# Kernel tuning notes

Measured on AMD Instinct MI355X. Metric: run time of the kernel, lower is better.

## Reference

```python
import jax, jax.numpy as jnp
import numpy as np

N_LAYERS = 3
N_NODES = 100000
N_EDGES = 1600000
D = 32


def setup_inputs() -> dict:
    key = jax.random.key(0)
    k1, k2, k3, k4 = jax.random.split(key, 4)
    edge_row = jax.random.randint(k1, (N_EDGES,), 0, N_NODES, dtype=jnp.int64 if jax.config.jax_enable_x64 else jnp.int32)
    edge_col = jax.random.randint(k2, (N_EDGES,), 0, N_NODES, dtype=edge_row.dtype)
    edge_val = jax.random.uniform(k3, (N_EDGES,), dtype=jnp.float32)
    x = jax.random.normal(k4, (N_NODES, D), dtype=jnp.float32)
    return {"edge_row": edge_row, "edge_col": edge_col, "edge_val": edge_val, "x": x}


def _spmm(edge_row, edge_col, edge_val, h):
    # y[r] = sum_{edges e with row r} val[e] * h[col[e]]  -- COO SpMM
    msgs = edge_val[:, None] * h[edge_col]  # [E, D]
    return jax.ops.segment_sum(msgs, edge_row, num_segments=N_NODES)


def reference(edge_row, edge_col, edge_val, x):
    # LightGCN propagation: mean over layer-0..n_layers embeddings
    out = x
    acc = x
    for _ in range(N_LAYERS):
        out = _spmm(edge_row, edge_col, edge_val, out)
        acc = acc + out
    return acc / jnp.asarray(N_LAYERS + 1, dtype=x.dtype)
```

## Files before the change

### kernel.cpp

```cpp
#include <hip/hip_runtime.h>


#define NN 100000
#define NE 1600000
#define DD 32
#define CHUNK 4096
#define NCHUNK ((NE + CHUNK - 1) / CHUNK)
#define BROWS 128
#define NBKT ((NN + BROWS - 1) / BROWS)
#define LDSE 3072

__device__ __forceinline__ unsigned f2bf(float f) {
    unsigned u = __float_as_uint(f);
    return (u + 0x7fffu + ((u >> 16) & 1u)) >> 16;
}


__global__ __launch_bounds__(1024) void hist_kernel(
    const int* __restrict__ row, int* __restrict__ H)
{
    __shared__ int cnt[NBKT];
    const int tid = threadIdx.x;
    const int start = blockIdx.x * CHUNK;
    const int n = min(CHUNK, NE - start);
    for (int k = tid; k < NBKT; k += 1024) cnt[k] = 0;
    __syncthreads();
    const int j = tid * 4;
    if (j + 3 < n) {
        int4 r4 = *(const int4*)(row + start + j);
        atomicAdd(&cnt[r4.x >> 7], 1);
        atomicAdd(&cnt[r4.y >> 7], 1);
        atomicAdd(&cnt[r4.z >> 7], 1);
        atomicAdd(&cnt[r4.w >> 7], 1);
    } else {
        for (int k = j; k < n; k++) atomicAdd(&cnt[row[start + k] >> 7], 1);
    }
    __syncthreads();
    int* Hrow = H + (size_t)blockIdx.x * NBKT;
    for (int k = tid; k < NBKT; k += 1024) Hrow[k] = cnt[k];
}


__global__ __launch_bounds__(1024) void scan_tr_kernel(
    const int* __restrict__ H, int* __restrict__ Pt, int* __restrict__ tot)
{
    const int b = blockIdx.x * 16 + (threadIdx.x >> 6);
    if (b >= NBKT) return;
    const int lane = threadIdx.x & 63;
    int run = 0;
    #pragma unroll
    for (int c0 = 0; c0 < NCHUNK; c0 += 64) {
        int c = c0 + lane;
        int v = (c < NCHUNK) ? H[(size_t)c * NBKT + b] : 0;
        int x = v;
        #pragma unroll
        for (int off = 1; off < 64; off <<= 1) {
            int y = __shfl_up(x, off, 64);
            if (lane >= off) x += y;
        }
        if (c < NCHUNK) Pt[(size_t)b * NCHUNK + c] = run + x - v;
        run += __shfl(x, 63, 64);
    }
    if (lane == 0) tot[b] = run;
}


__global__ __launch_bounds__(1024) void scan_buckets_kernel(
    const int* __restrict__ tot, int* __restrict__ bucketbase,
    int* __restrict__ row_ptr)
{
    const int tid = threadIdx.x;
    int v = (tid < NBKT) ? tot[tid] : 0;
    int lane = tid & 63, w = tid >> 6;
    int x = v;
    #pragma unroll
    for (int off = 1; off < 64; off <<= 1) {
        int y = __shfl_up(x, off, 64);
        if (lane >= off) x += y;
    }
    __shared__ int wt[16];
    if (lane == 63) wt[w] = x;
    __syncthreads();
    if (w == 0 && lane < 16) {
        int y = wt[lane];
        #pragma unroll
        for (int off = 1; off < 16; off <<= 1) {
            int z = __shfl_up(y, off, 16);
            if ((lane & 15) >= off) y += z;
        }
        wt[lane] = y;
    }
    __syncthreads();
    int wo = (w > 0) ? wt[w - 1] : 0;
    int excl = x + wo - v;
    if (tid < NBKT) bucketbase[tid] = excl;
    if (tid == NBKT) { bucketbase[NBKT] = NE; row_ptr[NN] = NE; }
}


__global__ __launch_bounds__(1024) void scatter_kernel(
    const int* __restrict__ row, const int* __restrict__ col,
    const float* __restrict__ val, const int* __restrict__ bucketbase,
    const int* __restrict__ Pt, int2* __restrict__ tmp)
{
    __shared__ int cnt[NBKT];
    __shared__ int lbase[NBKT];
    __shared__ int gofs[NBKT];
    __shared__ int wt[16];
    __shared__ int2 recs[CHUNK];
    __shared__ int dest[CHUNK];
    const int tid = threadIdx.x;
    const int start = blockIdx.x * CHUNK;
    const int n = min(CHUNK, NE - start);
    for (int k = tid; k < NBKT; k += 1024) cnt[k] = 0;
    __syncthreads();

    int rrow[CHUNK / 1024], rcol[CHUNK / 1024], rank[CHUNK / 1024];
    float rval[CHUNK / 1024];
    #pragma unroll
    for (int k = 0; k < CHUNK / 1024; k++) {
        int j = k * 1024 + tid;
        if (j < n) {
            int r = row[start + j];
            rrow[k] = r;
            rcol[k] = col[start + j];
            rval[k] = val[start + j];
            rank[k] = atomicAdd(&cnt[r >> 7], 1);
        } else {
            rrow[k] = -1;
        }
    }
    __syncthreads();

    int v = (tid < NBKT) ? cnt[tid] : 0;
    {
        int lane = tid & 63, w = tid >> 6;
        int x = v;
        #pragma unroll
        for (int off = 1; off < 64; off <<= 1) {
            int y = __shfl_up(x, off, 64);
            if (lane >= off) x += y;
        }
        if (lane == 63) wt[w] = x;
        __syncthreads();
        if (w == 0 && lane < 16) {
            int y = wt[lane];
            #pragma unroll
            for (int off = 1; off < 16; off <<= 1) {
                int z = __shfl_up(y, off, 16);
                if ((lane & 15) >= off) y += z;
            }
            wt[lane] = y;
        }
        __syncthreads();
        int excl = x + ((w > 0) ? wt[w - 1] : 0) - v;
        if (tid < NBKT) {
            lbase[tid] = excl;
            gofs[tid] = bucketbase[tid] + Pt[(size_t)tid * NCHUNK + blockIdx.x];
        }
    }
    __syncthreads();

    #pragma unroll
    for (int k = 0; k < CHUNK / 1024; k++) {
        if (rrow[k] >= 0) {
            int b = rrow[k] >> 7;
            int p = lbase[b] + rank[k];
            recs[p] = make_int2(((rrow[k] & 127) << 17) | rcol[k],
                                __float_as_int(rval[k]));
            dest[p] = gofs[b] + rank[k];
        }
    }
    __syncthreads();

    for (int p = tid; p < n; p += 1024)
        tmp[dest[p]] = recs[p];
}


__global__ __launch_bounds__(512) void bucket_sort_kernel(
    const int* __restrict__ bucketbase, const int2* __restrict__ tmp,
    int* __restrict__ row_ptr, int2* __restrict__ edges,
    int* __restrict__ rowperm)
{
    __shared__ int cntw[8][BROWS];
    __shared__ int curw[8][BROWS];
    __shared__ int base[BROWS];
    __shared__ int degsh[BROWS];
    __shared__ int wt2[2];
    __shared__ int2 ed[LDSE];
    const int tid = threadIdx.x;
    const int w   = tid >> 6;
    const int b   = blockIdx.x;
    const int s   = bucketbase[b];
    const int e   = bucketbase[b + 1];
    const int tot = e - s;

    for (int k = tid; k < 8 * BROWS; k += 512) (&cntw[0][0])[k] = 0;
    __syncthreads();

    int2 rc[6];
    #pragma unroll
    for (int k = 0; k < 6; k++) {
        int j = s + k * 512 + tid;
        rc[k] = (j < e && j < s + LDSE) ? tmp[j] : make_int2(-1, 0);
        if (rc[k].x >= 0) atomicAdd(&cntw[w][rc[k].x >> 17], 1);
    }
    if (tot > LDSE)
        for (int j = s + LDSE + tid; j < e; j += 512)
            atomicAdd(&cntw[w][tmp[j].x >> 17], 1);
    __syncthreads();

    int v = 0, x = 0;
    if (tid < BROWS) {
        int d = 0;
        #pragma unroll
        for (int ww = 0; ww < 8; ww++) d += cntw[ww][tid];
        degsh[tid] = d;
        v = d;
        int lane = tid & 63;
        x = v;
        #pragma unroll
        for (int off = 1; off < 64; off <<= 1) {
            int y = __shfl_up(x, off, 64);
            if (lane >= off) x += y;
        }
        if (lane == 63) wt2[tid >> 6] = x;
    }
    __syncthreads();
    if (tid < BROWS) {
        int excl = x + ((tid >> 6) ? wt2[0] : 0) - v;
        base[tid] = excl;
        int r = b * BROWS + tid;
        if (r < NN) row_ptr[r] = s + excl;
        int run = excl;
        #pragma unroll
        for (int ww = 0; ww < 8; ww++) { curw[ww][tid] = run; run += cntw[ww][tid]; }
        int half0 = tid & 64;
        int d = degsh[tid];
        int rank = 0;
        #pragma unroll 8
        for (int j2 = 0; j2 < 64; j2++) {
            int dj = degsh[half0 + j2];
            rank += (dj < d) || (dj == d && (half0 + j2) < tid);
        }
        rowperm[b * BROWS + half0 + rank] = b * BROWS + tid;
    }
    __syncthreads();

    if (tot <= LDSE) {
        #pragma unroll
        for (int k = 0; k < 6; k++) {
            if (rc[k].x >= 0) {
                int pos = atomicAdd(&curw[w][rc[k].x >> 17], 1);
                ed[pos] = make_int2(rc[k].x & 0x1FFFF, rc[k].y);
            }
        }
        __syncthreads();
        for (int k = tid; k < tot; k += 512)
            edges[s + k] = ed[k];
    } else {
        #pragma unroll
        for (int k = 0; k < 6; k++) {
            if (rc[k].x >= 0) {
                int pos = atomicAdd(&curw[w][rc[k].x >> 17], 1);
                edges[s + pos] = make_int2(rc[k].x & 0x1FFFF, rc[k].y);
            }
        }
        for (int j = s + LDSE + tid; j < e; j += 512) {
            int2 rec = tmp[j];
            int pos = atomicAdd(&curw[w][rec.x >> 17], 1);
            edges[s + pos] = make_int2(rec.x & 0x1FFFF, rec.y);
        }
    }
}


__global__ __launch_bounds__(256) void cvt_kernel(
    const float2* __restrict__ xin2, unsigned* __restrict__ hb)
{
    int j = blockIdx.x * 256 + threadIdx.x;
    if (j >= NN * DD / 2) return;
    float2 f = xin2[j];
    hb[j] = f2bf(f.x) | (f2bf(f.y) << 16);
}


template <int MODE>
__global__ __launch_bounds__(256) void spmm_kernel(
    const int* __restrict__ row_ptr, const int2* __restrict__ edges,
    const int* __restrict__ rowperm,
    const uint4* __restrict__ hb4,
    uint4* __restrict__ houtb4,
    const float4* __restrict__ xin4, float4* __restrict__ out4)
{
    const int g0 = blockIdx.x * 64 + (threadIdx.x >> 2);
    const int g = rowperm[g0];
    if (g >= NN) return;
    const int t = threadIdx.x & 3;
    const int s = row_ptr[g];
    const int e = row_ptr[g + 1];

    float acc[8] = {0.f, 0.f, 0.f, 0.f, 0.f, 0.f, 0.f, 0.f};

#define ACC8(W, V)                                                         \
    do {                                                                   \
        acc[0] += (V) * __uint_as_float((W).x << 16);                      \
        acc[1] += (V) * __uint_as_float((W).x & 0xffff0000u);              \
        acc[2] += (V) * __uint_as_float((W).y << 16);                      \
        acc[3] += (V) * __uint_as_float((W).y & 0xffff0000u);              \
        acc[4] += (V) * __uint_as_float((W).z << 16);                      \
        acc[5] += (V) * __uint_as_float((W).z & 0xffff0000u);              \
        acc[6] += (V) * __uint_as_float((W).w << 16);                      \
        acc[7] += (V) * __uint_as_float((W).w & 0xffff0000u);              \
    } while (0)

    int i = s;
    for (; i + 8 <= e; i += 8) {
        int2 a0 = edges[i];
        int2 a1 = edges[i + 1];
        int2 a2 = edges[i + 2];
        int2 a3 = edges[i + 3];
        int2 a4 = edges[i + 4];
        int2 a5 = edges[i + 5];
        int2 a6 = edges[i + 6];
        int2 a7 = edges[i + 7];
        uint4 w0 = hb4[a0.x * 4 + t];
        uint4 w1 = hb4[a1.x * 4 + t];
        uint4 w2 = hb4[a2.x * 4 + t];
        uint4 w3 = hb4[a3.x * 4 + t];
        uint4 w4 = hb4[a4.x * 4 + t];
        uint4 w5 = hb4[a5.x * 4 + t];
        uint4 w6 = hb4[a6.x * 4 + t];
        uint4 w7 = hb4[a7.x * 4 + t];
        ACC8(w0, __int_as_float(a0.y)); ACC8(w1, __int_as_float(a1.y));
        ACC8(w2, __int_as_float(a2.y)); ACC8(w3, __int_as_float(a3.y));
        ACC8(w4, __int_as_float(a4.y)); ACC8(w5, __int_as_float(a5.y));
        ACC8(w6, __int_as_float(a6.y)); ACC8(w7, __int_as_float(a7.y));
    }
    for (; i + 4 <= e; i += 4) {
        int2 a0 = edges[i];
        int2 a1 = edges[i + 1];
        int2 a2 = edges[i + 2];
        int2 a3 = edges[i + 3];
        uint4 w0 = hb4[a0.x * 4 + t];
        uint4 w1 = hb4[a1.x * 4 + t];
        uint4 w2 = hb4[a2.x * 4 + t];
        uint4 w3 = hb4[a3.x * 4 + t];
        ACC8(w0, __int_as_float(a0.y)); ACC8(w1, __int_as_float(a1.y));
        ACC8(w2, __int_as_float(a2.y)); ACC8(w3, __int_as_float(a3.y));
    }
    for (; i < e; ++i) {
        int2 a0 = edges[i];
        uint4 w0 = hb4[a0.x * 4 + t];
        ACC8(w0, __int_as_float(a0.y));
    }
#undef ACC8

    if (MODE == 0 || MODE == 1) {
        uint4 p;
        p.x = f2bf(acc[0]) | (f2bf(acc[1]) << 16);
        p.y = f2bf(acc[2]) | (f2bf(acc[3]) << 16);
        p.z = f2bf(acc[4]) | (f2bf(acc[5]) << 16);
        p.w = f2bf(acc[6]) | (f2bf(acc[7]) << 16);
        houtb4[g * 4 + t] = p;
    }
    const int o = g * 8 + t * 2;
    float4 lo, hi;
    if (MODE == 0) {
        float4 x0 = xin4[o], x1 = xin4[o + 1];
        lo = make_float4(x0.x + acc[0], x0.y + acc[1], x0.z + acc[2], x0.w + acc[3]);
        hi = make_float4(x1.x + acc[4], x1.y + acc[5], x1.z + acc[6], x1.w + acc[7]);
    } else if (MODE == 1) {
        float4 o0 = out4[o], o1 = out4[o + 1];
        lo = make_float4(o0.x + acc[0], o0.y + acc[1], o0.z + acc[2], o0.w + acc[3]);
        hi = make_float4(o1.x + acc[4], o1.y + acc[5], o1.z + acc[6], o1.w + acc[7]);
    } else {
        float4 o0 = out4[o], o1 = out4[o + 1];
        lo = make_float4((o0.x + acc[0]) * 0.25f, (o0.y + acc[1]) * 0.25f,
                         (o0.z + acc[2]) * 0.25f, (o0.w + acc[3]) * 0.25f);
        hi = make_float4((o1.x + acc[4]) * 0.25f, (o1.y + acc[5]) * 0.25f,
                         (o1.z + acc[6]) * 0.25f, (o1.w + acc[7]) * 0.25f);
    }
    out4[o] = lo;
    out4[o + 1] = hi;
}


extern "C" void kernel_launch(void* const* d_in, const int* in_sizes, int n_in,
                              void* d_out, int out_size, void* d_ws, size_t ws_size,
                              hipStream_t stream) {
    const int*   edge_row = (const int*)d_in[0];
    const int*   edge_col = (const int*)d_in[1];
    const float* edge_val = (const float*)d_in[2];
    const float* x        = (const float*)d_in[3];
    float* out = (float*)d_out;

    char* ws = (char*)d_ws;
    int*  H          = (int*)ws;   ws += (((size_t)NCHUNK * NBKT * 4) + 511) & ~511ull;
    int*  Pt         = (int*)ws;   ws += (((size_t)NBKT * NCHUNK * 4) + 511) & ~511ull;
    int*  tot        = (int*)ws;   ws += 4096;
    int*  bucketbase = (int*)ws;   ws += 4096;
    int*  row_ptr    = (int*)ws;   ws += ((size_t)(NN + 1) * 4 + 511) & ~511ull;
    int*  rowperm    = (int*)ws;   ws += (((size_t)NBKT * BROWS * 4) + 511) & ~511ull;
    int2* tmp        = (int2*)ws;  ws += (size_t)NE * 8 + 64;
    int2* edges      = (int2*)ws;  ws += (size_t)NE * 8 + 64;
    unsigned* hb0    = (unsigned*)ws;  ws += (size_t)NN * DD * 2;
    unsigned* hb1    = (unsigned*)ws;  ws += (size_t)NN * DD * 2;

    hist_kernel        <<<NCHUNK, 1024, 0, stream>>>(edge_row, H);
    scan_tr_kernel     <<<(NBKT + 15) / 16, 1024, 0, stream>>>(H, Pt, tot);
    scan_buckets_kernel<<<1, 1024, 0, stream>>>(tot, bucketbase, row_ptr);
    scatter_kernel     <<<NCHUNK, 1024, 0, stream>>>(edge_row, edge_col, edge_val,
                                                     bucketbase, Pt, tmp);
    bucket_sort_kernel <<<NBKT, 512, 0, stream>>>(bucketbase, tmp, row_ptr, edges,
                                                  rowperm);
    cvt_kernel         <<<(NN * DD / 2 + 255) / 256, 256, 0, stream>>>(
                         (const float2*)x, hb0);

    dim3 sp_grid((NN + 63) / 64);
    spmm_kernel<0><<<sp_grid, 256, 0, stream>>>(row_ptr, edges, rowperm,
        (const uint4*)hb0, (uint4*)hb1, (const float4*)x, (float4*)out);
    spmm_kernel<1><<<sp_grid, 256, 0, stream>>>(row_ptr, edges, rowperm,
        (const uint4*)hb1, (uint4*)hb0, (const float4*)x, (float4*)out);
    spmm_kernel<2><<<sp_grid, 256, 0, stream>>>(row_ptr, edges, rowperm,
        (const uint4*)hb0, (uint4*)hb1, (const float4*)x, (float4*)out);
}
```

Baseline: 199.3 us.

## Split bf16 features into two planes and run SpMM per half-feature plane

Stores the bf16 node features as two separate 16-feature planes and launches each SpMM layer twice, once per plane. Within a row, pairs of lanes now split the edges and combine partial sums with a cross-lane shuffle. The goal is a smaller gather working set per pass (a 3.2 MB plane) that fits better in cache. It also drops the per-bucket degree-sorted row permutation. In exchange the edge list is read twice per layer, the number of launches doubles, and half the lanes sit idle during the final writes.

Result: slower. 229.8 us (+15.3%).

```diff
diff --git a/kernel.cpp b/kernel.cpp
--- a/kernel.cpp
+++ b/kernel.cpp
@@ -9,6 +9,7 @@
 #define BROWS 128
 #define NBKT ((NN + BROWS - 1) / BROWS)
 #define LDSE 3072
+#define PLANE_U4 (NN * 2)
 
 __device__ __forceinline__ unsigned f2bf(float f) {
     unsigned u = __float_as_uint(f);
@@ -180,13 +181,10 @@
 
 __global__ __launch_bounds__(512) void bucket_sort_kernel(
     const int* __restrict__ bucketbase, const int2* __restrict__ tmp,
-    int* __restrict__ row_ptr, int2* __restrict__ edges,
-    int* __restrict__ rowperm)
+    int* __restrict__ row_ptr, int2* __restrict__ edges)
 {
     __shared__ int cntw[8][BROWS];
     __shared__ int curw[8][BROWS];
-    __shared__ int base[BROWS];
-    __shared__ int degsh[BROWS];
     __shared__ int wt2[2];
     __shared__ int2 ed[LDSE];
     const int tid = threadIdx.x;
@@ -216,7 +214,6 @@
         int d = 0;
         #pragma unroll
         for (int ww = 0; ww < 8; ww++) d += cntw[ww][tid];
-        degsh[tid] = d;
         v = d;
         int lane = tid & 63;
         x = v;
@@ -230,21 +227,11 @@
     __syncthreads();
     if (tid < BROWS) {
         int excl = x + ((tid >> 6) ? wt2[0] : 0) - v;
-        base[tid] = excl;
         int r = b * BROWS + tid;
         if (r < NN) row_ptr[r] = s + excl;
         int run = excl;
         #pragma unroll
         for (int ww = 0; ww < 8; ww++) { curw[ww][tid] = run; run += cntw[ww][tid]; }
-        int half0 = tid & 64;
-        int d = degsh[tid];
-        int rank = 0;
-        #pragma unroll 8
-        for (int j2 = 0; j2 < 64; j2++) {
-            int dj = degsh[half0 + j2];
-            rank += (dj < d) || (dj == d && (half0 + j2) < tid);
-        }
-        rowperm[b * BROWS + half0 + rank] = b * BROWS + tid;
     }
     __syncthreads();
 
@@ -280,24 +267,25 @@
     const float2* __restrict__ xin2, unsigned* __restrict__ hb)
 {
     int j = blockIdx.x * 256 + threadIdx.x;
-    if (j >= NN * DD / 2) return;
+    if (j >= NN * 16) return;
     float2 f = xin2[j];
-    hb[j] = f2bf(f.x) | (f2bf(f.y) << 16);
+    int nd = j >> 4, ff = j & 15;
+    hb[(ff >> 3) * (NN * 8) + nd * 8 + (ff & 7)] = f2bf(f.x) | (f2bf(f.y) << 16);
 }
 
 
 template <int MODE>
 __global__ __launch_bounds__(256) void spmm_kernel(
     const int* __restrict__ row_ptr, const int2* __restrict__ edges,
-    const int* __restrict__ rowperm,
-    const uint4* __restrict__ hb4,
-    uint4* __restrict__ houtb4,
-    const float4* __restrict__ xin4, float4* __restrict__ out4)
-{
-    const int g0 = blockIdx.x * 64 + (threadIdx.x >> 2);
-    const int g = rowperm[g0];
+    const uint4* __restrict__ hbp,
+    uint4* __restrict__ houtp,
+    const float4* __restrict__ xin4, float4* __restrict__ out4, int fo)
+{
+    const int g = blockIdx.x * 64 + (threadIdx.x >> 2);
     if (g >= NN) return;
-    const int t = threadIdx.x & 3;
+    const int t  = threadIdx.x & 3;
+    const int tp = t >> 1;
+    const int tc = t & 1;
     const int s = row_ptr[g];
     const int e = row_ptr[g + 1];
 
@@ -317,55 +305,42 @@
 
     int i = s;
     for (; i + 8 <= e; i += 8) {
-        int2 a0 = edges[i];
-        int2 a1 = edges[i + 1];
-        int2 a2 = edges[i + 2];
-        int2 a3 = edges[i + 3];
-        int2 a4 = edges[i + 4];
-        int2 a5 = edges[i + 5];
-        int2 a6 = edges[i + 6];
-        int2 a7 = edges[i + 7];
-        uint4 w0 = hb4[a0.x * 4 + t];
-        uint4 w1 = hb4[a1.x * 4 + t];
-        uint4 w2 = hb4[a2.x * 4 + t];
-        uint4 w3 = hb4[a3.x * 4 + t];
-        uint4 w4 = hb4[a4.x * 4 + t];
-        uint4 w5 = hb4[a5.x * 4 + t];
-        uint4 w6 = hb4[a6.x * 4 + t];
-        uint4 w7 = hb4[a7.x * 4 + t];
-        ACC8(w0, __int_as_float(a0.y)); ACC8(w1, __int_as_float(a1.y));
-        ACC8(w2, __int_as_float(a2.y)); ACC8(w3, __int_as_float(a3.y));
-        ACC8(w4, __int_as_float(a4.y)); ACC8(w5, __int_as_float(a5.y));
-        ACC8(w6, __int_as_float(a6.y)); ACC8(w7, __int_as_float(a7.y));
-    }
-    for (; i + 4 <= e; i += 4) {
-        int2 a0 = edges[i];
-        int2 a1 = edges[i + 1];
-        int2 a2 = edges[i + 2];
-        int2 a3 = edges[i + 3];
-        uint4 w0 = hb4[a0.x * 4 + t];
-        uint4 w1 = hb4[a1.x * 4 + t];
-        uint4 w2 = hb4[a2.x * 4 + t];
-        uint4 w3 = hb4[a3.x * 4 + t];
-        ACC8(w0, __int_as_float(a0.y)); ACC8(w1, __int_as_float(a1.y));
-        ACC8(w2, __int_as_float(a2.y)); ACC8(w3, __int_as_float(a3.y));
-    }
-    for (; i < e; ++i) {
-        int2 a0 = edges[i];
-        uint4 w0 = hb4[a0.x * 4 + t];
-        ACC8(w0, __int_as_float(a0.y));
+        int2 r0 = edges[i + 0 + tp];
+        int2 r1 = edges[i + 2 + tp];
+        int2 r2 = edges[i + 4 + tp];
+        int2 r3 = edges[i + 6 + tp];
+        uint4 w0 = hbp[r0.x * 2 + tc];
+        uint4 w1 = hbp[r1.x * 2 + tc];
+        uint4 w2 = hbp[r2.x * 2 + tc];
+        uint4 w3 = hbp[r3.x * 2 + tc];
+        ACC8(w0, __int_as_float(r0.y)); ACC8(w1, __int_as_float(r1.y));
+        ACC8(w2, __int_as_float(r2.y)); ACC8(w3, __int_as_float(r3.y));
+    }
+    for (; i + 2 <= e; i += 2) {
+        int2 r0 = edges[i + tp];
+        uint4 w0 = hbp[r0.x * 2 + tc];
+        ACC8(w0, __int_as_float(r0.y));
+    }
+    if (i < e && tp == 0) {
+        int2 r0 = edges[i];
+        uint4 w0 = hbp[r0.x * 2 + tc];
+        ACC8(w0, __int_as_float(r0.y));
     }
 #undef ACC8
 
+    #pragma unroll
+    for (int k = 0; k < 8; k++) acc[k] += __shfl_xor(acc[k], 2, 64);
+
+    if (t >= 2) return;
     if (MODE == 0 || MODE == 1) {
         uint4 p;
         p.x = f2bf(acc[0]) | (f2bf(acc[1]) << 16);
         p.y = f2bf(acc[2]) | (f2bf(acc[3]) << 16);
         p.z = f2bf(acc[4]) | (f2bf(acc[5]) << 16);
         p.w = f2bf(acc[6]) | (f2bf(acc[7]) << 16);
-        houtb4[g * 4 + t] = p;
-    }
-    const int o = g * 8 + t * 2;
+        houtp[g * 2 + t] = p;
+    }
+    const int o = g * 8 + fo * 4 + t * 2;
     float4 lo, hi;
     if (MODE == 0) {
         float4 x0 = xin4[o], x1 = xin4[o + 1];
@@ -402,7 +377,6 @@
     int*  tot        = (int*)ws;   ws += 4096;
     int*  bucketbase = (int*)ws;   ws += 4096;
     int*  row_ptr    = (int*)ws;   ws += ((size_t)(NN + 1) * 4 + 511) & ~511ull;
-    int*  rowperm    = (int*)ws;   ws += (((size_t)NBKT * BROWS * 4) + 511) & ~511ull;
     int2* tmp        = (int2*)ws;  ws += (size_t)NE * 8 + 64;
     int2* edges      = (int2*)ws;  ws += (size_t)NE * 8 + 64;
     unsigned* hb0    = (unsigned*)ws;  ws += (size_t)NN * DD * 2;
@@ -413,16 +387,26 @@
     scan_buckets_kernel<<<1, 1024, 0, stream>>>(tot, bucketbase, row_ptr);
     scatter_kernel     <<<NCHUNK, 1024, 0, stream>>>(edge_row, edge_col, edge_val,
                                                      bucketbase, Pt, tmp);
-    bucket_sort_kernel <<<NBKT, 512, 0, stream>>>(bucketbase, tmp, row_ptr, edges,
-                                                  rowperm);
-    cvt_kernel         <<<(NN * DD / 2 + 255) / 256, 256, 0, stream>>>(
+    bucket_sort_kernel <<<NBKT, 512, 0, stream>>>(bucketbase, tmp, row_ptr, edges);
+    cvt_kernel         <<<(NN * 16 + 255) / 256, 256, 0, stream>>>(
                          (const float2*)x, hb0);
 
+    const uint4* h0p0 = (const uint4*)hb0;
+    const uint4* h0p1 = (const uint4*)hb0 + PLANE_U4;
+    uint4*       h1p0 = (uint4*)hb1;
+    uint4*       h1p1 = (uint4*)hb1 + PLANE_U4;
+
     dim3 sp_grid((NN + 63) / 64);
-    spmm_kernel<0><<<sp_grid, 256, 0, stream>>>(row_ptr, edges, rowperm,
-        (const uint4*)hb0, (uint4*)hb1, (const float4*)x, (float4*)out);
-    spmm_kernel<1><<<sp_grid, 256, 0, stream>>>(row_ptr, edges, rowperm,
-        (const uint4*)hb1, (uint4*)hb0, (const float4*)x, (float4*)out);
-    spmm_kernel<2><<<sp_grid, 256, 0, stream>>>(row_ptr, edges, rowperm,
-        (const uint4*)hb0, (uint4*)hb1, (const float4*)x, (float4*)out);
-}
+    spmm_kernel<0><<<sp_grid, 256, 0, stream>>>(row_ptr, edges, h0p0, h1p0,
+        (const float4*)x, (float4*)out, 0);
+    spmm_kernel<0><<<sp_grid, 256, 0, stream>>>(row_ptr, edges, h0p1, h1p1,
+        (const float4*)x, (float4*)out, 1);
+    spmm_kernel<1><<<sp_grid, 256, 0, stream>>>(row_ptr, edges, h1p0, (uint4*)h0p0,
+        (const float4*)x, (float4*)out, 0);
+    spmm_kernel<1><<<sp_grid, 256, 0, stream>>>(row_ptr, edges, h1p1, (uint4*)h0p1,
+        (const float4*)x, (float4*)out, 1);
+    spmm_kernel<2><<<sp_grid, 256, 0, stream>>>(row_ptr, edges, h0p0, h1p0,
+        (const float4*)x, (float4*)out, 0);
+    spmm_kernel<2><<<sp_grid, 256, 0, stream>>>(row_ptr, edges, h0p1, h1p1,
+        (const float4*)x, (float4*)out, 1);
+}
```
